# Kernel tuning notes

Measured on AMD Instinct MI355X. Metric: run time of the kernel, lower is better.

The kernel has to match this reference:

```python
import jax, jax.numpy as jnp
import numpy as np

N_NODES = 50000
N_EDGES = 800000
D = 256


def setup_inputs() -> dict:
    key = jax.random.key(0)
    k_x, k_e, k_w1, k_w2 = jax.random.split(key, 4)
    x = jax.random.normal(k_x, (N_NODES, D), dtype=jnp.float32)
    edge_index = jax.random.randint(k_e, (2, N_EDGES), 0, N_NODES, dtype=jnp.int64)
    # attention MLP params (Linear(d, d//2) -> ReLU -> Linear(d//2, 1) -> Sigmoid)
    W1 = jax.random.normal(k_w1, (D, D // 2), dtype=jnp.float32) * (1.0 / np.sqrt(D))
    b1 = jnp.zeros((D // 2,), dtype=jnp.float32)
    W2 = jax.random.normal(k_w2, (D // 2, 1), dtype=jnp.float32) * (1.0 / np.sqrt(D // 2))
    b2 = jnp.zeros((1,), dtype=jnp.float32)
    return {"x": x, "edge_index": edge_index, "W1": W1, "b1": b1, "W2": W2, "b2": b2}


def reference(x, edge_index, W1, b1, W2, b2):
    # mean aggregation with attention: for each destination node i (row),
    # weighted mean of neighbor (col) features with sigmoid-MLP attention weights.
    row, col = edge_index[0], edge_index[1]
    neigh = x[col]                                   # [E, D] gathered neighbor features
    h = jax.nn.relu(neigh @ W1 + b1)                 # [E, D//2]
    w = jax.nn.sigmoid(h @ W2 + b2)                  # [E, 1] attention weight per edge
    num = jax.ops.segment_sum(neigh * w, row, num_segments=N_NODES)  # [N, D]
    den = jax.ops.segment_sum(w, row, num_segments=N_NODES)          # [N, 1]
    # nodes with no neighbors stay zero (matching the torch loop's skip)
    out = jnp.where(den > 0, num / jnp.maximum(den, 1e-12), 0.0)
    return out
```

## Files before the change

kernel.cpp:

```cpp
#include <hip/hip_runtime.h>
#include <hip/hip_bf16.h>

#define D 256
#define DH 128
#define NB 8

typedef __attribute__((ext_vector_type(8))) short short8;
typedef __attribute__((ext_vector_type(4))) float floatx4;
typedef __attribute__((ext_vector_type(4))) unsigned int uintx4;

__device__ __forceinline__ int eload(const void* p, long long i, int is64) {
    if (is64) return (int)((const long long*)p)[i];
    return ((const int*)p)[i];
}

__device__ __forceinline__ unsigned pack_bf16(unsigned a, unsigned b) {
    unsigned ra = (a + 0x7fffu + ((a >> 16) & 1u)) >> 16;
    unsigned rb = (b + 0x7fffu + ((b >> 16) & 1u)) & 0xffff0000u;
    return ra | rb;
}

__device__ __forceinline__ float4 unpack_bf16x4(uint2 v) {
    float4 r;
    r.x = __uint_as_float(v.x << 16);
    r.y = __uint_as_float(v.x & 0xffff0000u);
    r.z = __uint_as_float(v.y << 16);
    r.w = __uint_as_float(v.y & 0xffff0000u);
    return r;
}

__global__ __launch_bounds__(256) void prep_kernel(const float* __restrict__ W1,
                                                   uint4* __restrict__ Bp,
                                                   const int* __restrict__ ei,
                                                   int* __restrict__ flag, int E,
                                                   int* __restrict__ cursor,
                                                   int N, int pad) {
    if (blockIdx.x >= 17) {
        int stride = (gridDim.x - 17) * 256;
        int tid0 = (blockIdx.x - 17) * 256 + threadIdx.x;
        int total4 = (N * pad) >> 2;
        uint4* c4 = (uint4*)cursor;
        uint4 z = make_uint4(0u, 0u, 0u, 0u);
        for (int i = tid0; i < total4; i += stride) c4[i] = z;
        if (blockIdx.x == 17 && threadIdx.x == 0) {
            for (int i = total4 * 4; i < N * pad; ++i) cursor[i] = 0;
        }
        return;
    }
    if (blockIdx.x == 16) {
        int tid = threadIdx.x;
        if (tid == 0) *flag = 0;
        __syncthreads();
        int limit = min(E, 4096);
        int v = 0;
        for (int i = tid; i < limit; i += 256) v |= ei[2 * i + 1];
#pragma unroll
        for (int off = 32; off > 0; off >>= 1) v |= __shfl_down(v, off, 64);
        if ((tid & 63) == 0) atomicOr(flag, v);
        return;
    }
    int t = blockIdx.x * 256 + threadIdx.x;
    int lane = t & 63;
    int kt = (t >> 6) & 7;
    int nt = t >> 9;
    int col = nt * 16 + (lane & 15);
    int k0 = kt * 32 + (lane >> 4) * 8;
    unsigned v[8];
#pragma unroll
    for (int j = 0; j < 8; ++j) v[j] = __float_as_uint(W1[(k0 + j) * DH + col]);
    uint4 o;
    o.x = pack_bf16(v[0], v[1]);
    o.y = pack_bf16(v[2], v[3]);
    o.z = pack_bf16(v[4], v[5]);
    o.w = pack_bf16(v[6], v[7]);
    Bp[t] = o;
}

__global__ __launch_bounds__(256) void score_scatter_kernel(
        const float* __restrict__ x, const uint4* __restrict__ Bp,
        const float* __restrict__ b1, const float* __restrict__ W2,
        const float* __restrict__ b2, uint2* __restrict__ xb,
        float* __restrict__ s,
        const void* __restrict__ ep, const int* __restrict__ flag,
        int* __restrict__ cursor, unsigned short* __restrict__ cols,
        int cap, int pad, int Npad, int N, int E, int SB) {
    if ((int)blockIdx.x >= SB) {
        int is64 = (*flag == 0);
        int base = (blockIdx.x - SB) * 2048 + threadIdx.x;
        int r[8], c[8];
        bool vld[8];
#pragma unroll
        for (int j = 0; j < 8; ++j) {
            int e = base + j * 256;
            vld[j] = (e < E);
            if (vld[j]) {
                r[j] = eload(ep, e, is64);
                c[j] = eload(ep, (long long)E + e, is64);
            }
        }
#pragma unroll
        for (int j = 0; j < 8; ++j) {
            if (vld[j]) {
                int p = atomicAdd(&cursor[r[j] * pad], 1);
                if (p < cap)
                    __builtin_nontemporal_store((unsigned short)c[j],
                                                &cols[(size_t)r[j] * cap + p]);
            }
        }
        return;
    }

    int tid = threadIdx.x;
    int blk = blockIdx.x;
    long long n64 = (long long)N * 64;
    int npad8 = Npad * 8;

    long long gbase = (long long)blk * 4096 + tid;
#pragma unroll
    for (int i = 0; i < 16; ++i) {
        long long g = gbase + i * 256;
        int idx = i * 256 + tid;
        if (g < n64) {
            uint4 fv = ((const uint4*)x)[g];
            uint2 o;
            o.x = pack_bf16(fv.x, fv.y);
            o.y = pack_bf16(fv.z, fv.w);
            int row = idx >> 6, cc = idx & 63;
            int nodeid = blk * 64 + row;
            xb[(size_t)(cc >> 3) * npad8 + (size_t)nodeid * 8 + (cc & 7)] = o;
        }
    }
    __syncthreads();

    int lane = tid & 63;
    int wid = tid >> 6;
    int quad = lane >> 4;
    int rbase = blk * 64 + wid * 16;
    int lnode = rbase + (lane & 15);

    short8 afrag[8];
#pragma unroll
    for (int kt = 0; kt < 8; ++kt)
        afrag[kt] = *(const short8*)&xb[(size_t)kt * npad8 + (size_t)lnode * 8 + quad * 2];

    const short8* Bs = (const short8*)Bp;
    float z0 = 0.f, z1 = 0.f, z2 = 0.f, z3 = 0.f;
#pragma unroll
    for (int nt = 0; nt < 8; ++nt) {
        floatx4 acc = {0.f, 0.f, 0.f, 0.f};
#pragma unroll
        for (int kt = 0; kt < 8; ++kt) {
            short8 b = Bs[(nt * 8 + kt) * 64 + lane];
            acc = __builtin_amdgcn_mfma_f32_16x16x32_bf16(afrag[kt], b, acc, 0, 0, 0);
        }
        int col = nt * 16 + (lane & 15);
        float b1c = b1[col], w2c = W2[col];
        z0 += fmaxf(acc[0] + b1c, 0.f) * w2c;
        z1 += fmaxf(acc[1] + b1c, 0.f) * w2c;
        z2 += fmaxf(acc[2] + b1c, 0.f) * w2c;
        z3 += fmaxf(acc[3] + b1c, 0.f) * w2c;
    }

#pragma unroll
    for (int off = 1; off < 16; off <<= 1) {
        z0 += __shfl_xor(z0, off, 64);
        z1 += __shfl_xor(z1, off, 64);
        z2 += __shfl_xor(z2, off, 64);
        z3 += __shfl_xor(z3, off, 64);
    }
    if ((lane & 15) == 0) {
        float b2v = b2[0];
        int r = rbase + quad * 4;
        float zz[4] = {z0, z1, z2, z3};
#pragma unroll
        for (int j = 0; j < 4; ++j)
            if (r + j < N) s[r + j] = 1.f / (1.f + __expf(-(zz[j] + b2v)));
    }
}

__global__ __launch_bounds__(256) void agg_slice_kernel(
        const uint2* __restrict__ xb, const float* __restrict__ s,
        const int* __restrict__ cursor,
        const unsigned short* __restrict__ cols,
        int cap, int pad, int Npad, float4* __restrict__ out4, int N) {
    int slice = blockIdx.x & 7;
    int group = blockIdx.x >> 3;
    int wid  = threadIdx.x >> 6;
    int lane = threadIdx.x & 63;
    int g  = lane >> 3;
    int dl = lane & 7;
    int node = group * 32 + wid * 8 + g;
    bool alive = (node < N);

    int cnt = 0;
    if (alive) cnt = min(cursor[node * pad], cap);
    const unsigned short* mc = cols + (size_t)node * cap;
    const uint2* xbs = xb + (size_t)slice * Npad * 8;

    float4 acc = make_float4(0.f, 0.f, 0.f, 0.f);
    float den = 0.f;
    int k = 0;
    for (; k + 4 <= cnt; k += 4) {
        int c0 = mc[k], c1 = mc[k + 1], c2 = mc[k + 2], c3 = mc[k + 3];
        float s0 = s[c0], s1 = s[c1], s2 = s[c2], s3 = s[c3];
        uint2 v0 = xbs[(size_t)c0 * 8 + dl];
        uint2 v1 = xbs[(size_t)c1 * 8 + dl];
        uint2 v2 = xbs[(size_t)c2 * 8 + dl];
        uint2 v3 = xbs[(size_t)c3 * 8 + dl];
        float4 f0 = unpack_bf16x4(v0);
        float4 f1 = unpack_bf16x4(v1);
        float4 f2 = unpack_bf16x4(v2);
        float4 f3 = unpack_bf16x4(v3);
        acc.x = fmaf(f0.x, s0, fmaf(f1.x, s1, fmaf(f2.x, s2, fmaf(f3.x, s3, acc.x))));
        acc.y = fmaf(f0.y, s0, fmaf(f1.y, s1, fmaf(f2.y, s2, fmaf(f3.y, s3, acc.y))));
        acc.z = fmaf(f0.z, s0, fmaf(f1.z, s1, fmaf(f2.z, s2, fmaf(f3.z, s3, acc.z))));
        acc.w = fmaf(f0.w, s0, fmaf(f1.w, s1, fmaf(f2.w, s2, fmaf(f3.w, s3, acc.w))));
        den += (s0 + s1) + (s2 + s3);
    }
    for (; k < cnt; ++k) {
        int c0 = mc[k];
        float s0 = s[c0];
        float4 f0 = unpack_bf16x4(xbs[(size_t)c0 * 8 + dl]);
        acc.x = fmaf(f0.x, s0, acc.x);
        acc.y = fmaf(f0.y, s0, acc.y);
        acc.z = fmaf(f0.z, s0, acc.z);
        acc.w = fmaf(f0.w, s0, acc.w);
        den += s0;
    }
    if (alive) {
        floatx4 o = {0.f, 0.f, 0.f, 0.f};
        if (cnt > 0) {
            float inv = 1.f / den;
            o.x = acc.x * inv; o.y = acc.y * inv;
            o.z = acc.z * inv; o.w = acc.w * inv;
        }
        __builtin_nontemporal_store(
            o, (floatx4*)&out4[(size_t)node * 64 + slice * 8 + dl]);
    }
}

__global__ __launch_bounds__(256) void detect_kernel(const int* __restrict__ ei,
                                                     int* __restrict__ flag, int E) {
    int tid = threadIdx.x;
    int limit = min(E, 4096);
    int v = 0;
    for (int i = tid; i < limit; i += 256) v |= ei[2 * i + 1];
#pragma unroll
    for (int off = 32; off > 0; off >>= 1) v |= __shfl_down(v, off, 64);
    if ((tid & 63) == 0) atomicOr(flag, v);
}

__global__ __launch_bounds__(256) void score_kernel(const float* __restrict__ x,
                                                    const float* __restrict__ W1,
                                                    const float* __restrict__ b1,
                                                    const float* __restrict__ W2,
                                                    const float* __restrict__ b2,
                                                    float* __restrict__ s, int N) {
    __shared__ __align__(16) float xs[4][NB][D];
    int lane = threadIdx.x & 63;
    int wid  = threadIdx.x >> 6;
    int base = (blockIdx.x * 4 + wid) * NB;
#pragma unroll
    for (int m = 0; m < NB; ++m) {
        int n = base + m;
        float4 v = make_float4(0.f, 0.f, 0.f, 0.f);
        if (n < N) v = ((const float4*)x)[(size_t)n * 64 + lane];
        ((float4*)&xs[wid][m][0])[lane] = v;
    }
    __syncthreads();
    float h0[NB], h1[NB];
#pragma unroll
    for (int m = 0; m < NB; ++m) { h0[m] = 0.f; h1[m] = 0.f; }
#pragma unroll 4
    for (int k = 0; k < D; ++k) {
        float w1a = W1[k * DH + lane];
        float w1b = W1[k * DH + 64 + lane];
#pragma unroll
        for (int m = 0; m < NB; ++m) {
            float xv = xs[wid][m][k];
            h0[m] = fmaf(xv, w1a, h0[m]);
            h1[m] = fmaf(xv, w1b, h1[m]);
        }
    }
    float b1a = b1[lane], b1b = b1[lane + 64];
    float w2a = W2[lane], w2b = W2[lane + 64];
    float b2v = b2[0];
#pragma unroll
    for (int m = 0; m < NB; ++m) {
        float za = fmaxf(h0[m] + b1a, 0.f) * w2a + fmaxf(h1[m] + b1b, 0.f) * w2b;
#pragma unroll
        for (int off = 32; off > 0; off >>= 1) za += __shfl_down(za, off, 64);
        if (lane == 0) {
            int n = base + m;
            if (n < N) s[n] = 1.f / (1.f + __expf(-(za + b2v)));
        }
    }
}

__global__ __launch_bounds__(256) void hist_kernel(const void* __restrict__ ep,
                                                   const int* __restrict__ flag,
                                                   int* __restrict__ cnt, int E) {
    int is64 = (*flag == 0);
    int e = blockIdx.x * blockDim.x + threadIdx.x;
    if (e < E) atomicAdd(&cnt[eload(ep, e, is64)], 1);
}

__global__ __launch_bounds__(256) void bucket_kernel(const int* __restrict__ cnt,
                                                     int* __restrict__ beg,
                                                     int* __restrict__ cursor,
                                                     int* __restrict__ total, int N) {
    int i = blockIdx.x * blockDim.x + threadIdx.x;
    int lane = threadIdx.x & 63;
    int v = (i < N) ? cnt[i] : 0;
    int inc = v;
#pragma unroll
    for (int off = 1; off < 64; off <<= 1) {
        int t = __shfl_up(inc, off, 64);
        if (lane >= off) inc += t;
    }
    int base = 0;
    if (lane == 63) base = atomicAdd(total, inc);
    base = __shfl(base, 63, 64);
    if (i < N) {
        int b = base + inc - v;
        beg[i] = b;
        cursor[i] = b;
    }
}

__global__ __launch_bounds__(256) void scatter32_kernel(const void* __restrict__ ep,
                                                        const int* __restrict__ flag,
                                                        int* __restrict__ cursor,
                                                        int* __restrict__ cols, int E) {
    int is64 = (*flag == 0);
    int e = blockIdx.x * blockDim.x + threadIdx.x;
    if (e < E) {
        int r = eload(ep, e, is64);
        int c = eload(ep, (long long)E + e, is64);
        int p = atomicAdd(&cursor[r], 1);
        cols[p] = c;
    }
}

__global__ __launch_bounds__(256) void agg_f32_kernel(const float4* __restrict__ x4,
                                                      const float* __restrict__ s,
                                                      const int* __restrict__ begs,
                                                      const int* __restrict__ cnt,
                                                      const int* __restrict__ cols,
                                                      float4* __restrict__ out4, int N) {
    int lane = threadIdx.x & 63;
    int node = blockIdx.x * 4 + (threadIdx.x >> 6);
    if (node >= N) return;
    int beg = begs[node], end = beg + cnt[node];
    float4 acc = make_float4(0.f, 0.f, 0.f, 0.f);
    float den = 0.f;
    for (int k = beg; k < end; ++k) {
        int c = cols[k];
        float sc = s[c];
        float4 xv = x4[(size_t)c * 64 + lane];
        acc.x = fmaf(xv.x, sc, acc.x);
        acc.y = fmaf(xv.y, sc, acc.y);
        acc.z = fmaf(xv.z, sc, acc.z);
        acc.w = fmaf(xv.w, sc, acc.w);
        den += sc;
    }
    float4 o = make_float4(0.f, 0.f, 0.f, 0.f);
    if (end > beg) {
        float inv = 1.f / den;
        o.x = acc.x * inv; o.y = acc.y * inv; o.z = acc.z * inv; o.w = acc.w * inv;
    }
    out4[(size_t)node * 64 + lane] = o;
}

extern "C" void kernel_launch(void* const* d_in, const int* in_sizes, int n_in,
                              void* d_out, int out_size, void* d_ws, size_t ws_size,
                              hipStream_t stream) {
    const float* x  = (const float*)d_in[0];
    const void*  ei = d_in[1];
    const float* W1 = (const float*)d_in[2];
    const float* b1 = (const float*)d_in[3];
    const float* W2 = (const float*)d_in[4];
    const float* b2 = (const float*)d_in[5];
    int N = in_sizes[0] / D;
    int E = in_sizes[1] / 2;

    char* ws = (char*)d_ws;
    int Npad = (N + 63) & ~63;

    auto plan = [&](int cap, int pad, size_t& oCur, size_t& oS, size_t& oCols,
                    size_t& oBp, size_t& oXb) -> size_t {
        oCur  = 16;
        oS    = (oCur + (size_t)N * pad * 4 + 15) & ~15ull;
        oCols = (oS + (size_t)N * 4 + 255) & ~255ull;
        oBp   = (oCols + (size_t)N * cap * 2 + 255) & ~255ull;
        oXb   = (oBp + 65536 + 255) & ~255ull;
        return oXb + (size_t)Npad * D * 2;
    };

    int cap = 64, pad = 16;
    size_t oCur, oS, oCols, oBp, oXb;
    size_t need = plan(cap, pad, oCur, oS, oCols, oBp, oXb);
    if (need > ws_size) { pad = 4;  need = plan(cap, pad, oCur, oS, oCols, oBp, oXb); }
    if (need > ws_size) { pad = 1;  need = plan(cap, pad, oCur, oS, oCols, oBp, oXb); }

    if (N <= 65535 && need <= ws_size) {
        int*            flag   = (int*)(ws);
        int*            cursor = (int*)(ws + oCur);
        float*          s      = (float*)(ws + oS);
        unsigned short* cols   = (unsigned short*)(ws + oCols);
        uint4*          Bpack  = (uint4*)(ws + oBp);
        uint2*          xb     = (uint2*)(ws + oXb);

        const int ZB = 128;
        prep_kernel<<<17 + ZB, 256, 0, stream>>>(W1, Bpack, (const int*)ei, flag, E,
                                                 cursor, N, pad);

        int SB = (N + 63) / 64;
        int TBe = (E + 2047) / 2048;
        score_scatter_kernel<<<SB + TBe, 256, 0, stream>>>(x, Bpack, b1, W2, b2,
                                                           xb, s, ei, flag, cursor,
                                                           cols, cap, pad, Npad,
                                                           N, E, SB);
        int G32 = (N + 31) / 32;
        agg_slice_kernel<<<G32 * 8, 256, 0, stream>>>(xb, s, cursor, cols, cap, pad,
                                                      Npad, (float4*)d_out, N);
        return;
    }

    size_t o0 = 0;
    size_t o1 = 16;
    size_t o2 = (o1 + (size_t)N * 4 + 15) & ~15ull;
    size_t o3 = (o2 + (size_t)N * 4 + 15) & ~15ull;
    size_t o4 = (o3 + (size_t)N * 4 + 15) & ~15ull;
    size_t o5 = (o4 + (size_t)N * 4 + 15) & ~15ull;
    int*   flag   = (int*)(ws + o0);
    int*   total  = (int*)(ws + o0 + 4);
    int*   cnt    = (int*)(ws + o1);
    int*   beg    = (int*)(ws + o2);
    int*   cursor = (int*)(ws + o3);
    float* s      = (float*)(ws + o4);
    int*   cols   = (int*)(ws + o5);

    hipMemsetAsync(ws, 0, o1 + (size_t)N * 4, stream);
    detect_kernel<<<1, 256, 0, stream>>>((const int*)ei, flag, E);
    score_kernel<<<(N + 4 * NB - 1) / (4 * NB), 256, 0, stream>>>(x, W1, b1, W2, b2, s, N);
    hist_kernel<<<(E + 255) / 256, 256, 0, stream>>>(ei, flag, cnt, E);
    bucket_kernel<<<(N + 255) / 256, 256, 0, stream>>>(cnt, beg, cursor, total, N);
    scatter32_kernel<<<(E + 255) / 256, 256, 0, stream>>>(ei, flag, cursor, cols, E);
    agg_f32_kernel<<<(N + 3) / 4, 256, 0, stream>>>((const float4*)x, s, beg, cnt, cols,
                                                    (float4*)d_out, N);
}
```

Before: 227.5 us.

## Assign one node per wavefront in aggregation and split its edges across lane octets

The aggregation kernel now gives each wavefront a single destination node instead of eight. Its neighbor indices and attention scores are loaded cooperatively, one per lane, and broadcast with shuffles, while the eight lane-octets gather different edges in parallel before a cross-octet xor reduction. The aim is to remove per-lane serial edge loops and the divergence caused by uneven degrees within a wave, and to expose more memory-level parallelism. The cost is eight times as many blocks plus shuffle-reduction overhead. It also implicitly assumes at most 64 neighbors per node, since only 64 column entries are staged.

```diff
diff --git a/kernel.cpp b/kernel.cpp
--- a/kernel.cpp
+++ b/kernel.cpp
@@ -184,50 +184,52 @@
         const unsigned short* __restrict__ cols,
         int cap, int pad, int Npad, float4* __restrict__ out4, int N) {
     int slice = blockIdx.x & 7;
-    int group = blockIdx.x >> 3;
     int wid  = threadIdx.x >> 6;
     int lane = threadIdx.x & 63;
-    int g  = lane >> 3;
-    int dl = lane & 7;
-    int node = group * 32 + wid * 8 + g;
-    bool alive = (node < N);
-
-    int cnt = 0;
-    if (alive) cnt = min(cursor[node * pad], cap);
+    int oct = lane >> 3;
+    int dl  = lane & 7;
+    int node = (blockIdx.x >> 3) * 4 + wid;
+    if (node >= N) return;
+
+    int cnt = min(cursor[node * pad], cap);
     const unsigned short* mc = cols + (size_t)node * cap;
-    const uint2* xbs = xb + (size_t)slice * Npad * 8;
+
+    int ca = (lane < cnt) ? (int)mc[lane] : 0;
+    float sv_all = s[ca];
+    if (lane >= cnt) sv_all = 0.f;
+
+    const uint2* xbd = xb + (size_t)slice * Npad * 8 + dl;
 
     float4 acc = make_float4(0.f, 0.f, 0.f, 0.f);
     float den = 0.f;
-    int k = 0;
-    for (; k + 4 <= cnt; k += 4) {
-        int c0 = mc[k], c1 = mc[k + 1], c2 = mc[k + 2], c3 = mc[k + 3];
-        float s0 = s[c0], s1 = s[c1], s2 = s[c2], s3 = s[c3];
-        uint2 v0 = xbs[(size_t)c0 * 8 + dl];
-        uint2 v1 = xbs[(size_t)c1 * 8 + dl];
-        uint2 v2 = xbs[(size_t)c2 * 8 + dl];
-        uint2 v3 = xbs[(size_t)c3 * 8 + dl];
-        float4 f0 = unpack_bf16x4(v0);
-        float4 f1 = unpack_bf16x4(v1);
-        float4 f2 = unpack_bf16x4(v2);
-        float4 f3 = unpack_bf16x4(v3);
-        acc.x = fmaf(f0.x, s0, fmaf(f1.x, s1, fmaf(f2.x, s2, fmaf(f3.x, s3, acc.x))));
-        acc.y = fmaf(f0.y, s0, fmaf(f1.y, s1, fmaf(f2.y, s2, fmaf(f3.y, s3, acc.y))));
-        acc.z = fmaf(f0.z, s0, fmaf(f1.z, s1, fmaf(f2.z, s2, fmaf(f3.z, s3, acc.z))));
-        acc.w = fmaf(f0.w, s0, fmaf(f1.w, s1, fmaf(f2.w, s2, fmaf(f3.w, s3, acc.w))));
-        den += (s0 + s1) + (s2 + s3);
-    }
-    for (; k < cnt; ++k) {
-        int c0 = mc[k];
-        float s0 = s[c0];
-        float4 f0 = unpack_bf16x4(xbs[(size_t)c0 * 8 + dl]);
-        acc.x = fmaf(f0.x, s0, acc.x);
-        acc.y = fmaf(f0.y, s0, acc.y);
-        acc.z = fmaf(f0.z, s0, acc.z);
-        acc.w = fmaf(f0.w, s0, acc.w);
-        den += s0;
-    }
-    if (alive) {
+    int it = (cnt + 7) >> 3;
+    for (int i = 0; i < it; i += 2) {
+        int e0 = oct + 8 * i;
+        int e1 = (e0 + 8) & 63;
+        int   ce0 = __shfl(ca, e0, 64);
+        float sv0 = __shfl(sv_all, e0, 64);
+        int   ce1 = __shfl(ca, e1, 64);
+        float sv1 = __shfl(sv_all, e1, 64);
+        if (i + 1 >= it) sv1 = 0.f;
+        uint2 g0 = xbd[(size_t)ce0 * 8];
+        uint2 g1 = xbd[(size_t)ce1 * 8];
+        float4 f0 = unpack_bf16x4(g0);
+        float4 f1 = unpack_bf16x4(g1);
+        acc.x = fmaf(f0.x, sv0, fmaf(f1.x, sv1, acc.x));
+        acc.y = fmaf(f0.y, sv0, fmaf(f1.y, sv1, acc.y));
+        acc.z = fmaf(f0.z, sv0, fmaf(f1.z, sv1, acc.z));
+        acc.w = fmaf(f0.w, sv0, fmaf(f1.w, sv1, acc.w));
+        den += sv0 + sv1;
+    }
+#pragma unroll
+    for (int off = 8; off < 64; off <<= 1) {
+        acc.x += __shfl_xor(acc.x, off, 64);
+        acc.y += __shfl_xor(acc.y, off, 64);
+        acc.z += __shfl_xor(acc.z, off, 64);
+        acc.w += __shfl_xor(acc.w, off, 64);
+        den   += __shfl_xor(den,   off, 64);
+    }
+    if (oct == 0) {
         floatx4 o = {0.f, 0.f, 0.f, 0.f};
         if (cnt > 0) {
             float inv = 1.f / den;
@@ -421,9 +423,9 @@
                                                            xb, s, ei, flag, cursor,
                                                            cols, cap, pad, Npad,
                                                            N, E, SB);
-        int G32 = (N + 31) / 32;
-        agg_slice_kernel<<<G32 * 8, 256, 0, stream>>>(xb, s, cursor, cols, cap, pad,
-                                                      Npad, (float4*)d_out, N);
+        int G4 = (N + 3) / 4;
+        agg_slice_kernel<<<G4 * 8, 256, 0, stream>>>(xb, s, cursor, cols, cap, pad,
+                                                     Npad, (float4*)d_out, N);
         return;
     }
 
```

Result: slower. 276.1 us (+21.3%).
